# Optimization experiments

Hardware: AMD Instinct MI355X
Metric: run time of the kernel (lower is better)

## Reference

```python
import jax, jax.numpy as jnp
import numpy as np

N = 50000      # nodes
F_IN = 1024    # raw feature dim
D = 64         # student_dim = hidden_dim * compression_ratio
P = 3          # number of meta-paths
E = 1600000    # edges per meta-path adjacency (avg degree 32)


def setup_inputs() -> dict:
    key = jax.random.key(0)
    ks = jax.random.split(key, 10)
    feats = jax.random.normal(ks[0], (N, F_IN), jnp.float32)
    rows = jax.random.randint(ks[1], (P, E), 0, N, dtype=jnp.int32)
    cols = jax.random.randint(ks[2], (P, E), 0, N, dtype=jnp.int32)
    # normalized-adjacency-like positive edge weights
    vals = jax.random.uniform(ks[3], (P, E), jnp.float32) / 32.0
    # fc_list[0]: Linear(F_IN -> D), xavier_normal gain=1.414
    W0 = jax.random.normal(ks[4], (D, F_IN), jnp.float32) * 0.05
    b0 = jnp.zeros((D,), jnp.float32)
    # P GCN linear layers (D -> D, no bias) + GCN bias params
    Wg = jax.random.normal(ks[5], (P, D, D), jnp.float32) * 0.17
    bg = jnp.zeros((P, D), jnp.float32)
    # PReLU alpha (torch default init 0.25, one scalar per GCN)
    alpha = jnp.full((P,), 0.25, jnp.float32)
    # Attention: Linear(D -> D) and att vector [1, D]
    Wa = jax.random.normal(ks[6], (D, D), jnp.float32) * 0.17
    ba = jnp.zeros((D,), jnp.float32)
    att = jax.random.normal(ks[7], (1, D), jnp.float32) * 0.17
    return dict(feats=feats, rows=rows, cols=cols, vals=vals, W0=W0, b0=b0,
                Wg=Wg, bg=bg, alpha=alpha, Wa=Wa, ba=ba, att=att)


def reference(feats, rows, cols, vals, W0, b0, Wg, bg, alpha, Wa, ba, att):
    # h = elu(fc_list[0](feats))  (feat_drop = 0 -> identity)
    h = jax.nn.elu(feats @ W0.T + b0)                       # [N, D]
    embeds = []
    for i in range(P):
        s = h @ Wg[i].T                                     # [N, D]
        # sparse adj (COO) @ s : out[r] += v * s[c]
        msg = vals[i][:, None] * s[cols[i]]                 # [E, D]
        out = jax.ops.segment_sum(msg, rows[i], num_segments=N)
        out = out + bg[i]
        embeds.append(jnp.where(out > 0, out, alpha[i] * out))  # PReLU
    emb = jnp.stack(embeds)                                 # [P, N, D]
    # Attention over views: beta_i = att . mean_n tanh(fc(emb_i))
    sp = jnp.tanh(jnp.einsum('pnd,ed->pne', emb, Wa) + ba).mean(axis=1)  # [P, D]
    beta = jax.nn.softmax(sp @ att[0])                      # [P]
    z_mp = jnp.einsum('p,pnd->nd', beta, emb)               # [N, D]
    return z_mp
```

## Files before the change

kernel.cpp:

```cpp
#include <hip/hip_runtime.h>
#include <hip/hip_bf16.h>

#define N_NODES 50000
#define F_IN    1024
#define DD      64
#define PP      3
#define EE      1600000
#define NPC     98
#define CCAP    17664
#define NB1     391
#define P1B     625

typedef __attribute__((ext_vector_type(8))) short short8v;
typedef __attribute__((ext_vector_type(4))) float floatx4;
typedef __attribute__((ext_vector_type(2))) float floatx2;

__device__ inline float bfl(uint u) { return __uint_as_float(u << 16); }
__device__ inline float bfh(uint u) { return __uint_as_float(u & 0xffff0000u); }
__device__ inline floatx2 up2(uint u) {
    floatx2 r; r.x = bfl(u); r.y = bfh(u); return r;
}
__device__ inline uint cvtpk2(float a, float b) {
    __hip_bfloat162 h = __float22bfloat162_rn(make_float2(a, b));
    return *(uint*)&h;
}
__device__ inline ushort f2bf(float x) {
    __hip_bfloat16 h = __float2bfloat16(x);
    return *(ushort*)&h;
}

__global__ __launch_bounds__(256) void split_weights(const float* __restrict__ W0,
                                                     const float* __restrict__ Wg,
                                                     const float* __restrict__ Wa,
                                                     ushort* __restrict__ W0h,
                                                     ushort* __restrict__ Wgh,
                                                     ushort* __restrict__ Wah)
{
    int i = blockIdx.x * 256 + threadIdx.x;
    if (i < 64 * 1024) W0h[i] = f2bf(W0[i]);
    int j = i - 64 * 1024;
    if (j >= 0 && j < PP * 64 * 64) Wgh[j] = f2bf(Wg[j]);
    int k = i - 64 * 1024 - PP * 64 * 64;
    if (k >= 0 && k < 64 * 64) Wah[k] = f2bf(Wa[k]);
}

__global__ __launch_bounds__(512) void fused_front(const float* __restrict__ feats,
                                                   const ushort* __restrict__ W0h,
                                                   float* __restrict__ hpart,
                                                   const int*   __restrict__ rows,
                                                   const int*   __restrict__ cols,
                                                   const float* __restrict__ vals,
                                                   int*   __restrict__ pcur3,
                                                   uint2* __restrict__ coarsebuf)
{
    __shared__ __align__(16) char smem[43008];
    const int t = threadIdx.x;

    if (blockIdx.x < 4 * NB1) {
        ushort* Bh = (ushort*)smem;
        const int blk = blockIdx.x;
        const int kq = blk / NB1;
        const int bx = blk % NB1;
        const int w = t >> 6, lane = t & 63;
        const int row0 = bx * 128;
        const int l15 = lane & 15, l4 = lane >> 4;

        #pragma unroll
        for (int rep = 0; rep < 4; ++rep) {
            int id = rep * 512 + t;
            int d = id >> 5, uu = id & 31;
            *(uint4*)&Bh[d * 256 + ((uu ^ (d & 7)) << 3)] =
                *(const uint4*)&W0h[(size_t)d * F_IN + kq * 256 + uu * 8];
        }
        __syncthreads();

        int gr = row0 + w * 16 + l15;
        if (gr >= N_NODES) gr = N_NODES - 1;
        const float* arow = feats + (size_t)gr * F_IN + kq * 256 + l4 * 8;

        floatx4 acc[4] = {};
        #pragma unroll 4
        for (int ks = 0; ks < 8; ++ks) {
            float4 a0 = *(const float4*)&arow[ks * 32];
            float4 a1 = *(const float4*)&arow[ks * 32 + 4];
            uint4 av;
            av.x = cvtpk2(a0.x, a0.y); av.y = cvtpk2(a0.z, a0.w);
            av.z = cvtpk2(a1.x, a1.y); av.w = cvtpk2(a1.z, a1.w);
            short8v ah = *(short8v*)&av;
            int u = ks * 4 + l4;
            #pragma unroll
            for (int cf = 0; cf < 4; ++cf) {
                int d = cf * 16 + l15;
                short8v bh = *(short8v*)&Bh[d * 256 + ((u ^ (d & 7)) << 3)];
                acc[cf] = __builtin_amdgcn_mfma_f32_16x16x32_bf16(ah, bh, acc[cf], 0, 0, 0);
            }
        }

        float* hp = hpart + ((size_t)(kq * NB1 + bx)) * 8192;
        #pragma unroll
        for (int cf = 0; cf < 4; ++cf)
            *(float4*)&hp[(cf * 512 + t) * 4] = make_float4(acc[cf][0], acc[cf][1],
                                                            acc[cf][2], acc[cf][3]);
    } else {
        uint2* stage  = (uint2*)smem;
        uint2* sorted = (uint2*)(smem + 20480);
        int*   cnt    = (int*)(smem + 40960);
        int*   sc     = (int*)(smem + 41472);
        int*   curb   = (int*)(smem + 41984);
        int*   gbase  = (int*)(smem + 42496);

        const int pidx = blockIdx.x - 4 * NB1;
        const int path = pidx / P1B;
        const int bx   = pidx % P1B;
        const size_t ebase = (size_t)path * EE + (size_t)bx * 2560;
        int* pcur = pcur3 + path * NPC;
        uint2* cb = coarsebuf + (size_t)path * NPC * CCAP;

        if (t < 128) { cnt[t] = 0; curb[t] = 0; }
        __syncthreads();

        #pragma unroll
        for (int it = 0; it < 5; ++it) {
            int e = it * 512 + t;
            int r = rows[ebase + e];
            int c = cols[ebase + e];
            float v = vals[ebase + e];
            int bin = r >> 9, rl = r & 511;
            stage[e] = make_uint2((uint)c | ((uint)rl << 16) | ((uint)bin << 25),
                                  __float_as_uint(v));
            atomicAdd(&cnt[bin], 1);
        }
        __syncthreads();

        if (t < 128) sc[t] = cnt[t];
        __syncthreads();
        #pragma unroll
        for (int o = 1; o < 128; o <<= 1) {
            int v = (t < 128 && t >= o) ? sc[t - o] : 0;
            __syncthreads();
            if (t < 128 && t >= o) sc[t] += v;
            __syncthreads();
        }

        if (t < NPC) gbase[t] = atomicAdd(&pcur[t], cnt[t]);
        __syncthreads();

        #pragma unroll
        for (int it = 0; it < 5; ++it) {
            uint2 e = stage[it * 512 + t];
            int bin = e.x >> 25;
            int loc = (sc[bin] - cnt[bin]) + atomicAdd(&curb[bin], 1);
            sorted[loc] = e;
        }
        __syncthreads();

        #pragma unroll
        for (int it = 0; it < 5; ++it) {
            int i = it * 512 + t;
            uint2 e = sorted[i];
            int bin = e.x >> 25;
            int g = gbase[bin] + (i - (sc[bin] - cnt[bin]));
            if (g < CCAP) cb[(size_t)bin * CCAP + g] = e;
        }
    }
}

__global__ __launch_bounds__(256) void gemm2_combine(const float* __restrict__ hpart,
                                                     const float* __restrict__ b0,
                                                     const ushort* __restrict__ Wgh,
                                                     ushort* __restrict__ s_all)
{
    __shared__ ushort Ah[64 * 64];
    __shared__ ushort Bh[64 * 64];
    __shared__ ushort Sout[64 * 64];
    const int t = threadIdx.x;
    const int w = t >> 6, lane = t & 63;
    const int row0 = blockIdx.x * 64;
    const int bi = blockIdx.x >> 1;
    const int hh = blockIdx.x & 1;
    const int l15 = lane & 15, l4 = lane >> 4;

    #pragma unroll
    for (int cf = 0; cf < 4; ++cf) {
        int idx = (cf * 512 + hh * 256 + t) * 4;
        float4 a = *(const float4*)&hpart[(size_t)bi * 8192 + idx];
        float4 b = *(const float4*)&hpart[((size_t)NB1 + bi) * 8192 + idx];
        float4 c = *(const float4*)&hpart[((size_t)2 * NB1 + bi) * 8192 + idx];
        float4 d = *(const float4*)&hpart[((size_t)3 * NB1 + bi) * 8192 + idx];
        int col = cf * 16 + l15;
        float bias = b0[col];
        float xs[4] = {a.x + b.x + c.x + d.x + bias, a.y + b.y + c.y + d.y + bias,
                       a.z + b.z + c.z + d.z + bias, a.w + b.w + c.w + d.w + bias};
        #pragma unroll
        for (int r = 0; r < 4; ++r) {
            int row = w * 16 + l4 * 4 + r;
            float x = xs[r];
            x = x > 0.f ? x : (__expf(x) - 1.f);
            int u = (col >> 3) ^ (row & 7);
            Ah[row * 64 + u * 8 + (col & 7)] = f2bf(x);
        }
    }
    __syncthreads();

    for (int p = 0; p < PP; ++p) {
        #pragma unroll
        for (int rep = 0; rep < 2; ++rep) {
            int idx = rep * 256 + t;
            int r = idx >> 3, u8 = idx & 7;
            int unit = u8 ^ (r & 7);
            *(uint4*)&Bh[r * 64 + unit * 8] = *(const uint4*)&Wgh[(size_t)p * 4096 + idx * 8];
        }
        __syncthreads();

        floatx4 sacc[4] = {};
        #pragma unroll
        for (int ks = 0; ks < 2; ++ks) {
            int arow2 = w * 16 + l15;
            int au = (ks * 4 + l4) ^ (arow2 & 7);
            short8v ah = *(short8v*)&Ah[arow2 * 64 + au * 8];
            #pragma unroll
            for (int cf = 0; cf < 4; ++cf) {
                int bcol = cf * 16 + l15;
                int bu = (ks * 4 + l4) ^ (bcol & 7);
                short8v bh = *(short8v*)&Bh[bcol * 64 + bu * 8];
                sacc[cf] = __builtin_amdgcn_mfma_f32_16x16x32_bf16(ah, bh, sacc[cf], 0, 0, 0);
            }
        }
        #pragma unroll
        for (int cf = 0; cf < 4; ++cf) {
            int col = cf * 16 + l15;
            #pragma unroll
            for (int r = 0; r < 4; ++r)
                Sout[(w * 16 + l4 * 4 + r) * 64 + col] = f2bf(sacc[cf][r]);
        }
        __syncthreads();
        {
            int lr = t >> 2;
            int gr = row0 + lr;
            if (gr < N_NODES) {
                ushort* sp = s_all + (size_t)p * N_NODES * 64;
                int co = (t & 3) * 16;
                *(uint4*)&sp[(size_t)gr * 64 + co]     = *(uint4*)&Sout[lr * 64 + co];
                *(uint4*)&sp[(size_t)gr * 64 + co + 8] = *(uint4*)&Sout[lr * 64 + co + 8];
            }
        }
        __syncthreads();
    }
}

__global__ __launch_bounds__(512) void sort2(const uint2* __restrict__ coarsebuf,
                                             const int*   __restrict__ pcur3,
                                             uint* __restrict__ sortpk,
                                             int* __restrict__ rowbeg3,
                                             int* __restrict__ rowend3)
{
    __shared__ int hist[512];
    __shared__ int cur[512];
    const int t = threadIdx.x;
    const int c = blockIdx.x, path = blockIdx.y;
    const int n = min(pcur3[path * NPC + c], CCAP);
    const size_t slabbase = ((size_t)path * NPC + c) * CCAP;
    const uint2* src = coarsebuf + slabbase;

    hist[t] = 0;
    __syncthreads();

    for (int i = t; i < n; i += 512)
        atomicAdd(&hist[(src[i].x >> 16) & 511], 1);
    __syncthreads();

    int c0 = hist[t];
    __syncthreads();
    #pragma unroll
    for (int o = 1; o < 512; o <<= 1) {
        int v = (t >= o) ? hist[t - o] : 0;
        __syncthreads();
        hist[t] += v;
        __syncthreads();
    }
    int excl = hist[t] - c0;
    cur[t] = excl;
    int gr = c * 512 + t;
    if (gr < N_NODES) {
        rowbeg3[path * N_NODES + gr] = (int)(slabbase + excl);
        rowend3[path * N_NODES + gr] = (int)(slabbase + excl + c0);
    }
    __syncthreads();

    for (int i = t; i < n; i += 512) {
        uint2 e = src[i];
        int rl = (e.x >> 16) & 511;
        int pos = atomicAdd(&cur[rl], 1);
        sortpk[slabbase + pos] = (e.x & 0xffffu) |
                                 ((uint)f2bf(__uint_as_float(e.y)) << 16);
    }
}

__global__ __launch_bounds__(256) void spmm_gather(const uint*   __restrict__ sortpk,
                                                   const int*    __restrict__ rowbeg3,
                                                   const int*    __restrict__ rowend3,
                                                   const ushort* __restrict__ s_all,
                                                   const float*  __restrict__ bg,
                                                   const float*  __restrict__ alpha,
                                                   ushort* __restrict__ emb)
{
    const int path = blockIdx.x / 12500;
    const int wid = (blockIdx.x % 12500) * 4 + (threadIdx.x >> 6);
    const int lane = threadIdx.x & 63;
    const int dq = lane & 7;
    const int slot = lane >> 3;
    const int e0 = rowbeg3[path * N_NODES + wid];
    const int e1 = rowend3[path * N_NODES + wid];
    const ushort* s_p = s_all + (size_t)path * N_NODES * 64;

    floatx2 acc[4] = {};
    if (e0 < e1) {
        const int last = e1 - 1;
        for (int e = e0; e < e1; e += 32) {
            int ea = e + slot, eb = ea + 8, ec = ea + 16, ed = ea + 24;
            uint pka = sortpk[min(ea, last)];
            uint pkb = sortpk[min(eb, last)];
            uint pkc = sortpk[min(ec, last)];
            uint pkd = sortpk[min(ed, last)];
            const uint4 ga = *(const uint4*)&s_p[(size_t)(pka & 0xffffu) * 64 + dq * 8];
            const uint4 gb = *(const uint4*)&s_p[(size_t)(pkb & 0xffffu) * 64 + dq * 8];
            const uint4 gc = *(const uint4*)&s_p[(size_t)(pkc & 0xffffu) * 64 + dq * 8];
            const uint4 gd = *(const uint4*)&s_p[(size_t)(pkd & 0xffffu) * 64 + dq * 8];
            float va = (ea <= last) ? bfh(pka) : 0.f;
            float vb = (eb <= last) ? bfh(pkb) : 0.f;
            float vc = (ec <= last) ? bfh(pkc) : 0.f;
            float vd = (ed <= last) ? bfh(pkd) : 0.f;
            floatx2 va2 = {va, va}, vb2 = {vb, vb}, vc2 = {vc, vc}, vd2 = {vd, vd};
            acc[0] += va2 * up2(ga.x); acc[1] += va2 * up2(ga.y);
            acc[2] += va2 * up2(ga.z); acc[3] += va2 * up2(ga.w);
            acc[0] += vb2 * up2(gb.x); acc[1] += vb2 * up2(gb.y);
            acc[2] += vb2 * up2(gb.z); acc[3] += vb2 * up2(gb.w);
            acc[0] += vc2 * up2(gc.x); acc[1] += vc2 * up2(gc.y);
            acc[2] += vc2 * up2(gc.z); acc[3] += vc2 * up2(gc.w);
            acc[0] += vd2 * up2(gd.x); acc[1] += vd2 * up2(gd.y);
            acc[2] += vd2 * up2(gd.z); acc[3] += vd2 * up2(gd.w);
        }
    }
    #pragma unroll
    for (int j = 0; j < 4; ++j) {
        acc[j].x += __shfl_xor(acc[j].x, 8);
        acc[j].y += __shfl_xor(acc[j].y, 8);
        acc[j].x += __shfl_xor(acc[j].x, 16);
        acc[j].y += __shfl_xor(acc[j].y, 16);
        acc[j].x += __shfl_xor(acc[j].x, 32);
        acc[j].y += __shfl_xor(acc[j].y, 32);
    }

    if (slot == 0) {
        const float al = alpha[path];
        const float* bgp = bg + path * 64;
        float x[8];
        #pragma unroll
        for (int j = 0; j < 4; ++j) {
            float v0 = acc[j].x + bgp[dq * 8 + 2 * j];
            float v1 = acc[j].y + bgp[dq * 8 + 2 * j + 1];
            x[2 * j]     = v0 > 0.f ? v0 : al * v0;
            x[2 * j + 1] = v1 > 0.f ? v1 : al * v1;
        }
        uint4 wv;
        wv.x = cvtpk2(x[0], x[1]);
        wv.y = cvtpk2(x[2], x[3]);
        wv.z = cvtpk2(x[4], x[5]);
        wv.w = cvtpk2(x[6], x[7]);
        *(uint4*)&emb[((size_t)path * N_NODES + wid) * 64 + dq * 8] = wv;
    }
}

__global__ __launch_bounds__(256) void postproc(const ushort* __restrict__ emb,
                                                const ushort* __restrict__ Wah,
                                                const float* __restrict__ ba,
                                                float* __restrict__ sp)
{
    __shared__ ushort Ah[64 * 64];
    __shared__ ushort Bh[64 * 64];
    __shared__ float red[16][64];
    const int t = threadIdx.x;
    const int w = t >> 6, lane = t & 63;
    const int l15 = lane & 15, l4 = lane >> 4;
    const int nb = (N_NODES + 63) >> 6;
    const int p  = blockIdx.x / nb;
    const int tb = blockIdx.x % nb;
    const int row0 = tb * 64;
    const ushort* embp = emb + (size_t)p * N_NODES * 64;

    #pragma unroll
    for (int rep = 0; rep < 2; ++rep) {
        int idx = rep * 256 + t;
        int r = idx >> 3, u8 = idx & 7;
        int gr = row0 + r; if (gr >= N_NODES) gr = N_NODES - 1;
        int unit = u8 ^ (r & 7);
        *(uint4*)&Ah[r * 64 + unit * 8] = *(const uint4*)&embp[(size_t)gr * 64 + u8 * 8];
        *(uint4*)&Bh[r * 64 + unit * 8] = *(const uint4*)&Wah[idx * 8];
    }
    __syncthreads();

    floatx4 acc[4] = {};
    #pragma unroll
    for (int ks = 0; ks < 2; ++ks) {
        int arow = w * 16 + l15;
        int au = (ks * 4 + l4) ^ (arow & 7);
        short8v ah = *(short8v*)&Ah[arow * 64 + au * 8];
        #pragma unroll
        for (int cf = 0; cf < 4; ++cf) {
            int bcol = cf * 16 + l15;
            int bu = (ks * 4 + l4) ^ (bcol & 7);
            short8v bh = *(short8v*)&Bh[bcol * 64 + bu * 8];
            acc[cf] = __builtin_amdgcn_mfma_f32_16x16x32_bf16(ah, bh, acc[cf], 0, 0, 0);
        }
    }

    #pragma unroll
    for (int cf = 0; cf < 4; ++cf) {
        int col = cf * 16 + l15;
        float s = 0.f;
        #pragma unroll
        for (int r = 0; r < 4; ++r) {
            int gr = row0 + w * 16 + l4 * 4 + r;
            if (gr < N_NODES) s += tanhf(acc[cf][r] + ba[col]);
        }
        red[w * 4 + l4][col] = s;
    }
    __syncthreads();
    if (t < 64) {
        float ssum = 0.f;
        #pragma unroll
        for (int g = 0; g < 16; ++g) ssum += red[g][t];
        unsafeAtomicAdd(&sp[p * 64 + t], ssum);
    }
}

__global__ void beta_kernel(const float* __restrict__ sp,
                            const float* __restrict__ att,
                            float* __restrict__ beta)
{
    int lane = threadIdx.x;
    float w[PP];
    #pragma unroll
    for (int p = 0; p < PP; ++p) {
        float x = sp[p * 64 + lane] * (1.0f / (float)N_NODES) * att[lane];
        #pragma unroll
        for (int off = 32; off; off >>= 1) x += __shfl_down(x, off);
        w[p] = __shfl(x, 0);
    }
    if (lane == 0) {
        float mx = fmaxf(w[0], fmaxf(w[1], w[2]));
        float e0 = __expf(w[0] - mx);
        float e1 = __expf(w[1] - mx);
        float e2 = __expf(w[2] - mx);
        float s = e0 + e1 + e2;
        beta[0] = e0 / s; beta[1] = e1 / s; beta[2] = e2 / s;
    }
}

__global__ __launch_bounds__(256) void combine(const ushort* __restrict__ emb,
                                               const float* __restrict__ beta,
                                               float* __restrict__ out)
{
    const float b0 = beta[0], b1 = beta[1], b2 = beta[2];
    const size_t tot = (size_t)N_NODES * 64;
    size_t i = ((size_t)blockIdx.x * 256 + threadIdx.x) * 8;
    if (i < tot) {
        uint4 e0 = *(const uint4*)&emb[i];
        uint4 e1 = *(const uint4*)&emb[tot + i];
        uint4 e2 = *(const uint4*)&emb[2 * tot + i];
        float o[8];
        o[0] = b0*bfl(e0.x) + b1*bfl(e1.x) + b2*bfl(e2.x);
        o[1] = b0*bfh(e0.x) + b1*bfh(e1.x) + b2*bfh(e2.x);
        o[2] = b0*bfl(e0.y) + b1*bfl(e1.y) + b2*bfl(e2.y);
        o[3] = b0*bfh(e0.y) + b1*bfh(e1.y) + b2*bfh(e2.y);
        o[4] = b0*bfl(e0.z) + b1*bfl(e1.z) + b2*bfl(e2.z);
        o[5] = b0*bfh(e0.z) + b1*bfh(e1.z) + b2*bfh(e2.z);
        o[6] = b0*bfl(e0.w) + b1*bfl(e1.w) + b2*bfl(e2.w);
        o[7] = b0*bfh(e0.w) + b1*bfh(e1.w) + b2*bfh(e2.w);
        *(float4*)&out[i]     = make_float4(o[0], o[1], o[2], o[3]);
        *(float4*)&out[i + 4] = make_float4(o[4], o[5], o[6], o[7]);
    }
}

extern "C" void kernel_launch(void* const* d_in, const int* in_sizes, int n_in,
                              void* d_out, int out_size, void* d_ws, size_t ws_size,
                              hipStream_t stream)
{
    const float* feats = (const float*)d_in[0];
    const int*   rows  = (const int*)  d_in[1];
    const int*   cols  = (const int*)  d_in[2];
    const float* vals  = (const float*)d_in[3];
    const float* W0    = (const float*)d_in[4];
    const float* b0    = (const float*)d_in[5];
    const float* Wg    = (const float*)d_in[6];
    const float* bg    = (const float*)d_in[7];
    const float* alpha = (const float*)d_in[8];
    const float* Wa    = (const float*)d_in[9];
    const float* ba    = (const float*)d_in[10];
    const float* att   = (const float*)d_in[11];
    float* out = (float*)d_out;

    const size_t ND = (size_t)N_NODES * 64;
    char* base = (char*)d_ws;
    ushort* emb    = (ushort*)base;              base += 3 * ND * 2;
    ushort* s_all  = (ushort*)base;              base += 3 * ND * 2;
    ushort* W0h    = (ushort*)base;              base += 64 * 1024 * 2;
    ushort* Wgh    = (ushort*)base;              base += PP * 64 * 64 * 2;
    ushort* Wah    = (ushort*)base;              base += 64 * 64 * 2;
    int*    pcur3  = (int*)base;                 base += PP * NPC * 4;
    float*  sp     = (float*)base;               base += 192 * 4;
    float*  beta   = (float*)base;               base += 64 * 4;
    int*    rowbeg3 = (int*)base;                base += PP * N_NODES * 4;
    int*    rowend3 = (int*)base;                base += PP * N_NODES * 4;
    base = (char*)(((size_t)base + 255) & ~(size_t)255);
    float*  hpart  = (float*)base;               base += (size_t)4 * NB1 * 8192 * 4;
    uint2*  coarsebuf = (uint2*)base;            base += (size_t)PP * NPC * CCAP * 8;
    uint*   sortpk    = (uint*)base;             base += (size_t)PP * NPC * CCAP * 4;

    hipMemsetAsync(pcur3, 0, (PP * NPC + 192) * sizeof(int), stream);

    split_weights<<<(64 * 1024 + PP * 64 * 64 + 64 * 64 + 255) / 256, 256, 0, stream>>>(
        W0, Wg, Wa, W0h, Wgh, Wah);

    fused_front<<<4 * NB1 + 3 * P1B, 512, 0, stream>>>(
        feats, W0h, hpart, rows, cols, vals, pcur3, coarsebuf);

    gemm2_combine<<<782, 256, 0, stream>>>(hpart, b0, Wgh, s_all);
    sort2<<<dim3(NPC, 3), 512, 0, stream>>>(coarsebuf, pcur3, sortpk, rowbeg3, rowend3);
    spmm_gather<<<3 * 12500, 256, 0, stream>>>(
        sortpk, rowbeg3, rowend3, s_all, bg, alpha, emb);

    postproc<<<3 * 782, 256, 0, stream>>>(emb, Wah, ba, sp);
    beta_kernel<<<1, 64, 0, stream>>>(sp, att, beta);
    combine<<<(int)((ND / 8 + 255) / 256), 256, 0, stream>>>(emb, beta, out);
}
```

Baseline: 290.1 us.

## Interleave GEMM and partition blocks; fuse gemm2 and sort2 into one launch

In the front kernel, GEMM blocks and edge-partition blocks are now interleaved (even/odd block IDs) so memory-bound partitioning overlaps compute-bound MFMA work on the same CUs. The second-layer GEMM and the per-bin sort are merged into a single kernel, with 512-thread GEMM blocks each handling 128 rows, so one launch and its tail drain are removed and the two phases run concurrently. The cost is a larger shared-memory footprint per block and possible imbalance between the heterogeneous block types.

```diff
diff --git a/kernel.cpp b/kernel.cpp
--- a/kernel.cpp
+++ b/kernel.cpp
@@ -10,6 +10,8 @@
 #define CCAP    17664
 #define NB1     391
 #define P1B     625
+#define GEMM1B  (4 * NB1)
+#define PART1B  (3 * P1B)
 
 typedef __attribute__((ext_vector_type(8))) short short8v;
 typedef __attribute__((ext_vector_type(4))) float floatx4;
@@ -55,10 +57,12 @@
 {
     __shared__ __align__(16) char smem[43008];
     const int t = threadIdx.x;
-
-    if (blockIdx.x < 4 * NB1) {
+    const int bid = blockIdx.x;
+    const bool is_gemm = (bid < 2 * GEMM1B) && ((bid & 1) == 0);
+
+    if (is_gemm) {
         ushort* Bh = (ushort*)smem;
-        const int blk = blockIdx.x;
+        const int blk = bid >> 1;
         const int kq = blk / NB1;
         const int bx = blk % NB1;
         const int w = t >> 6, lane = t & 63;
@@ -109,7 +113,7 @@
         int*   curb   = (int*)(smem + 41984);
         int*   gbase  = (int*)(smem + 42496);
 
-        const int pidx = blockIdx.x - 4 * NB1;
+        const int pidx = (bid < 2 * GEMM1B) ? (bid >> 1) : (bid - GEMM1B);
         const int path = pidx / P1B;
         const int bx   = pidx % P1B;
         const size_t ebase = (size_t)path * EE + (size_t)bx * 2560;
@@ -165,134 +169,139 @@
     }
 }
 
-__global__ __launch_bounds__(256) void gemm2_combine(const float* __restrict__ hpart,
-                                                     const float* __restrict__ b0,
-                                                     const ushort* __restrict__ Wgh,
-                                                     ushort* __restrict__ s_all)
-{
-    __shared__ ushort Ah[64 * 64];
-    __shared__ ushort Bh[64 * 64];
-    __shared__ ushort Sout[64 * 64];
+__global__ __launch_bounds__(512) void fused_mid(const float* __restrict__ hpart,
+                                                 const float* __restrict__ b0,
+                                                 const ushort* __restrict__ Wgh,
+                                                 ushort* __restrict__ s_all,
+                                                 const uint2* __restrict__ coarsebuf,
+                                                 const int*   __restrict__ pcur3,
+                                                 uint* __restrict__ sortpk,
+                                                 int* __restrict__ rowbeg3,
+                                                 int* __restrict__ rowend3)
+{
+    __shared__ __align__(16) char smem[40960];
     const int t = threadIdx.x;
-    const int w = t >> 6, lane = t & 63;
-    const int row0 = blockIdx.x * 64;
-    const int bi = blockIdx.x >> 1;
-    const int hh = blockIdx.x & 1;
-    const int l15 = lane & 15, l4 = lane >> 4;
-
-    #pragma unroll
-    for (int cf = 0; cf < 4; ++cf) {
-        int idx = (cf * 512 + hh * 256 + t) * 4;
-        float4 a = *(const float4*)&hpart[(size_t)bi * 8192 + idx];
-        float4 b = *(const float4*)&hpart[((size_t)NB1 + bi) * 8192 + idx];
-        float4 c = *(const float4*)&hpart[((size_t)2 * NB1 + bi) * 8192 + idx];
-        float4 d = *(const float4*)&hpart[((size_t)3 * NB1 + bi) * 8192 + idx];
-        int col = cf * 16 + l15;
-        float bias = b0[col];
-        float xs[4] = {a.x + b.x + c.x + d.x + bias, a.y + b.y + c.y + d.y + bias,
-                       a.z + b.z + c.z + d.z + bias, a.w + b.w + c.w + d.w + bias};
-        #pragma unroll
-        for (int r = 0; r < 4; ++r) {
-            int row = w * 16 + l4 * 4 + r;
-            float x = xs[r];
-            x = x > 0.f ? x : (__expf(x) - 1.f);
-            int u = (col >> 3) ^ (row & 7);
-            Ah[row * 64 + u * 8 + (col & 7)] = f2bf(x);
-        }
-    }
-    __syncthreads();
-
-    for (int p = 0; p < PP; ++p) {
-        #pragma unroll
-        for (int rep = 0; rep < 2; ++rep) {
-            int idx = rep * 256 + t;
-            int r = idx >> 3, u8 = idx & 7;
-            int unit = u8 ^ (r & 7);
-            *(uint4*)&Bh[r * 64 + unit * 8] = *(const uint4*)&Wgh[(size_t)p * 4096 + idx * 8];
-        }
-        __syncthreads();
-
-        floatx4 sacc[4] = {};
-        #pragma unroll
-        for (int ks = 0; ks < 2; ++ks) {
-            int arow2 = w * 16 + l15;
-            int au = (ks * 4 + l4) ^ (arow2 & 7);
-            short8v ah = *(short8v*)&Ah[arow2 * 64 + au * 8];
+    const int bid = blockIdx.x;
+
+    if (bid < NB1) {
+        ushort* Ah   = (ushort*)smem;
+        ushort* Bh   = (ushort*)(smem + 16384);
+        ushort* Sout = (ushort*)(smem + 24576);
+        const int sub = t >> 8;
+        const int tt  = t & 255;
+        const int w = tt >> 6, lane = tt & 63;
+        const int l15 = lane & 15, l4 = lane >> 4;
+        const int bi = bid;
+        const int row0 = bi * 128 + sub * 64;
+        ushort* Ahs = Ah + sub * 4096;
+        ushort* Souts = Sout + sub * 4096;
+
+        #pragma unroll
+        for (int cf = 0; cf < 4; ++cf) {
+            int idx = (cf * 512 + sub * 256 + tt) * 4;
+            float4 a = *(const float4*)&hpart[(size_t)bi * 8192 + idx];
+            float4 b = *(const float4*)&hpart[((size_t)NB1 + bi) * 8192 + idx];
+            float4 c = *(const float4*)&hpart[((size_t)2 * NB1 + bi) * 8192 + idx];
+            float4 d = *(const float4*)&hpart[((size_t)3 * NB1 + bi) * 8192 + idx];
+            int col = cf * 16 + l15;
+            float bias = b0[col];
+            float xs[4] = {a.x + b.x + c.x + d.x + bias, a.y + b.y + c.y + d.y + bias,
+                           a.z + b.z + c.z + d.z + bias, a.w + b.w + c.w + d.w + bias};
+            #pragma unroll
+            for (int r = 0; r < 4; ++r) {
+                int row = w * 16 + l4 * 4 + r;
+                float x = xs[r];
+                x = x > 0.f ? x : (__expf(x) - 1.f);
+                int u = (col >> 3) ^ (row & 7);
+                Ahs[row * 64 + u * 8 + (col & 7)] = f2bf(x);
+            }
+        }
+        __syncthreads();
+
+        for (int p = 0; p < PP; ++p) {
+            {
+                int r = t >> 3, u8 = t & 7;
+                int unit = u8 ^ (r & 7);
+                *(uint4*)&Bh[r * 64 + unit * 8] =
+                    *(const uint4*)&Wgh[(size_t)p * 4096 + t * 8];
+            }
+            __syncthreads();
+
+            floatx4 sacc[4] = {};
+            #pragma unroll
+            for (int ks = 0; ks < 2; ++ks) {
+                int arow2 = w * 16 + l15;
+                int au = (ks * 4 + l4) ^ (arow2 & 7);
+                short8v ah = *(short8v*)&Ahs[arow2 * 64 + au * 8];
+                #pragma unroll
+                for (int cf = 0; cf < 4; ++cf) {
+                    int bcol = cf * 16 + l15;
+                    int bu = (ks * 4 + l4) ^ (bcol & 7);
+                    short8v bh = *(short8v*)&Bh[bcol * 64 + bu * 8];
+                    sacc[cf] = __builtin_amdgcn_mfma_f32_16x16x32_bf16(ah, bh, sacc[cf], 0, 0, 0);
+                }
+            }
             #pragma unroll
             for (int cf = 0; cf < 4; ++cf) {
-                int bcol = cf * 16 + l15;
-                int bu = (ks * 4 + l4) ^ (bcol & 7);
-                short8v bh = *(short8v*)&Bh[bcol * 64 + bu * 8];
-                sacc[cf] = __builtin_amdgcn_mfma_f32_16x16x32_bf16(ah, bh, sacc[cf], 0, 0, 0);
+                int col = cf * 16 + l15;
+                #pragma unroll
+                for (int r = 0; r < 4; ++r)
+                    Souts[(w * 16 + l4 * 4 + r) * 64 + col] = f2bf(sacc[cf][r]);
             }
-        }
-        #pragma unroll
-        for (int cf = 0; cf < 4; ++cf) {
-            int col = cf * 16 + l15;
-            #pragma unroll
-            for (int r = 0; r < 4; ++r)
-                Sout[(w * 16 + l4 * 4 + r) * 64 + col] = f2bf(sacc[cf][r]);
-        }
-        __syncthreads();
-        {
-            int lr = t >> 2;
-            int gr = row0 + lr;
-            if (gr < N_NODES) {
-                ushort* sp = s_all + (size_t)p * N_NODES * 64;
-                int co = (t & 3) * 16;
-                *(uint4*)&sp[(size_t)gr * 64 + co]     = *(uint4*)&Sout[lr * 64 + co];
-                *(uint4*)&sp[(size_t)gr * 64 + co + 8] = *(uint4*)&Sout[lr * 64 + co + 8];
+            __syncthreads();
+            {
+                int lr = tt >> 2;
+                int gr = row0 + lr;
+                if (gr < N_NODES) {
+                    ushort* sp = s_all + (size_t)p * N_NODES * 64;
+                    int co = (tt & 3) * 16;
+                    *(uint4*)&sp[(size_t)gr * 64 + co]     = *(uint4*)&Souts[lr * 64 + co];
+                    *(uint4*)&sp[(size_t)gr * 64 + co + 8] = *(uint4*)&Souts[lr * 64 + co + 8];
+                }
             }
-        }
-        __syncthreads();
-    }
-}
-
-__global__ __launch_bounds__(512) void sort2(const uint2* __restrict__ coarsebuf,
-                                             const int*   __restrict__ pcur3,
-                                             uint* __restrict__ sortpk,
-                                             int* __restrict__ rowbeg3,
-                                             int* __restrict__ rowend3)
-{
-    __shared__ int hist[512];
-    __shared__ int cur[512];
-    const int t = threadIdx.x;
-    const int c = blockIdx.x, path = blockIdx.y;
-    const int n = min(pcur3[path * NPC + c], CCAP);
-    const size_t slabbase = ((size_t)path * NPC + c) * CCAP;
-    const uint2* src = coarsebuf + slabbase;
-
-    hist[t] = 0;
-    __syncthreads();
-
-    for (int i = t; i < n; i += 512)
-        atomicAdd(&hist[(src[i].x >> 16) & 511], 1);
-    __syncthreads();
-
-    int c0 = hist[t];
-    __syncthreads();
-    #pragma unroll
-    for (int o = 1; o < 512; o <<= 1) {
-        int v = (t >= o) ? hist[t - o] : 0;
-        __syncthreads();
-        hist[t] += v;
-        __syncthreads();
-    }
-    int excl = hist[t] - c0;
-    cur[t] = excl;
-    int gr = c * 512 + t;
-    if (gr < N_NODES) {
-        rowbeg3[path * N_NODES + gr] = (int)(slabbase + excl);
-        rowend3[path * N_NODES + gr] = (int)(slabbase + excl + c0);
-    }
-    __syncthreads();
-
-    for (int i = t; i < n; i += 512) {
-        uint2 e = src[i];
-        int rl = (e.x >> 16) & 511;
-        int pos = atomicAdd(&cur[rl], 1);
-        sortpk[slabbase + pos] = (e.x & 0xffffu) |
-                                 ((uint)f2bf(__uint_as_float(e.y)) << 16);
+            __syncthreads();
+        }
+    } else {
+        int* hist = (int*)smem;
+        int* cur  = (int*)(smem + 2048);
+        const int sidx = bid - NB1;
+        const int c = sidx % NPC, path = sidx / NPC;
+        const int n = min(pcur3[path * NPC + c], CCAP);
+        const size_t slabbase = ((size_t)path * NPC + c) * CCAP;
+        const uint2* src = coarsebuf + slabbase;
+
+        hist[t] = 0;
+        __syncthreads();
+
+        for (int i = t; i < n; i += 512)
+            atomicAdd(&hist[(src[i].x >> 16) & 511], 1);
+        __syncthreads();
+
+        int c0 = hist[t];
+        __syncthreads();
+        #pragma unroll
+        for (int o = 1; o < 512; o <<= 1) {
+            int v = (t >= o) ? hist[t - o] : 0;
+            __syncthreads();
+            hist[t] += v;
+            __syncthreads();
+        }
+        int excl = hist[t] - c0;
+        cur[t] = excl;
+        int gr = c * 512 + t;
+        if (gr < N_NODES) {
+            rowbeg3[path * N_NODES + gr] = (int)(slabbase + excl);
+            rowend3[path * N_NODES + gr] = (int)(slabbase + excl + c0);
+        }
+        __syncthreads();
+
+        for (int i = t; i < n; i += 512) {
+            uint2 e = src[i];
+            int rl = (e.x >> 16) & 511;
+            int pos = atomicAdd(&cur[rl], 1);
+            sortpk[slabbase + pos] = (e.x & 0xffffu) |
+                                     ((uint)f2bf(__uint_as_float(e.y)) << 16);
+        }
     }
 }
 
@@ -522,11 +531,12 @@
     split_weights<<<(64 * 1024 + PP * 64 * 64 + 64 * 64 + 255) / 256, 256, 0, stream>>>(
         W0, Wg, Wa, W0h, Wgh, Wah);
 
-    fused_front<<<4 * NB1 + 3 * P1B, 512, 0, stream>>>(
+    fused_front<<<GEMM1B + PART1B, 512, 0, stream>>>(
         feats, W0h, hpart, rows, cols, vals, pcur3, coarsebuf);
 
-    gemm2_combine<<<782, 256, 0, stream>>>(hpart, b0, Wgh, s_all);
-    sort2<<<dim3(NPC, 3), 512, 0, stream>>>(coarsebuf, pcur3, sortpk, rowbeg3, rowend3);
+    fused_mid<<<NB1 + 3 * NPC, 512, 0, stream>>>(
+        hpart, b0, Wgh, s_all, coarsebuf, pcur3, sortpk, rowbeg3, rowend3);
+
     spmm_gather<<<3 * 12500, 256, 0, stream>>>(
         sortpk, rowbeg3, rowend3, s_all, bg, alpha, emb);
 
```

After: 274.4 us (median of 2 runs). -5.4%, faster.
